# Performance work log

Hardware: AMD Instinct MI355X
Metric: run time of the kernel (lower is better)

Reference implementation:

```python
import jax, jax.numpy as jnp
import numpy as np

DIM, SSM, RNN = 1024, 64, 128


def setup_inputs() -> dict:
    key = jax.random.key(0)
    ks = jax.random.split(key, 16)
    s = 0.02
    B, N = 8, 2048
    return {
        'x': jax.random.normal(ks[0], (B, N, DIM), jnp.float32),
        'A': jax.random.normal(ks[1], (SSM, SSM), jnp.float32) * s,
        'Bw': jax.random.normal(ks[2], (SSM, DIM), jnp.float32) * s,
        'Bb': jnp.zeros((SSM,), jnp.float32),
        'Cw': jax.random.normal(ks[3], (DIM, SSM), jnp.float32) * s,
        'Cb': jnp.zeros((DIM,), jnp.float32),
        'Dw': jax.random.normal(ks[4], (DIM, DIM), jnp.float32) * s,
        'Db': jnp.zeros((DIM,), jnp.float32),
        'W_ih': jax.random.normal(ks[5], (3 * RNN, DIM), jnp.float32) * s,
        'b_ih': jnp.zeros((3 * RNN,), jnp.float32),
        'W_hh': jax.random.normal(ks[6], (3 * RNN, RNN), jnp.float32) * s,
        'b_hh': jnp.zeros((3 * RNN,), jnp.float32),
        'proj_w': jax.random.normal(ks[7], (DIM, RNN), jnp.float32) * s,
        'proj_b': jnp.zeros((DIM,), jnp.float32),
        'gate_w': jax.random.normal(ks[8], (2, DIM), jnp.float32) * s,
        'gate_b': jnp.zeros((2,), jnp.float32),
    }


def reference(x, A, Bw, Bb, Cw, Cb, Dw, Db, W_ih, b_ih, W_hh, b_hh, proj_w, proj_b, gate_w, gate_b):
    B, N, D = x.shape
    R = W_hh.shape[1]
    # Precompute all input-side projections once (time-parallel GEMMs).
    bx = jnp.einsum('bnd,sd->bns', x, Bw) + Bb            # [B,N,SSM]
    dx = jnp.einsum('bnd,ed->bne', x, Dw) + Db            # [B,N,D]
    gx = jax.nn.sigmoid(jnp.einsum('bnd,gd->bng', x, gate_w) + gate_b)  # [B,N,2]
    ih = jnp.einsum('bnd,rd->bnr', x, W_ih) + b_ih        # [B,N,3R]
    # time-major for scan
    bx_t = jnp.swapaxes(bx, 0, 1)
    dx_t = jnp.swapaxes(dx, 0, 1)
    gx_t = jnp.swapaxes(gx, 0, 1)
    ih_t = jnp.swapaxes(ih, 0, 1)

    h_ssm0 = jnp.zeros((B, A.shape[0]), x.dtype)
    h_rnn0 = jnp.zeros((B, R), x.dtype)

    def step(carry, inp):
        h_ssm, h_rnn = carry
        bxt, dxt, gxt, iht = inp
        h_ssm = jax.nn.silu(h_ssm @ A.T + bxt)
        y_ssm = h_ssm @ Cw.T + Cb + dxt
        # GRUCell (torch semantics)
        hh = h_rnn @ W_hh.T + b_hh
        i_r, i_z, i_n = jnp.split(iht, 3, axis=-1)
        h_r, h_z, h_n = jnp.split(hh, 3, axis=-1)
        r = jax.nn.sigmoid(i_r + h_r)
        z = jax.nn.sigmoid(i_z + h_z)
        n = jnp.tanh(i_n + r * h_n)
        h_rnn = (1.0 - z) * n + z * h_rnn
        y_rnn = h_rnn @ proj_w.T + proj_b
        fused = gxt[:, :1] * y_ssm + gxt[:, 1:2] * y_rnn
        return (h_ssm, h_rnn), fused

    _, out = jax.lax.scan(step, (h_ssm0, h_rnn0), (bx_t, dx_t, gx_t, ih_t))
    return jnp.swapaxes(out, 0, 1)  # [B,N,D]
```

## Files before the change

kernel.cpp:

```cpp
#include <hip/hip_runtime.h>


#define MROWS 16384
#define SEQ   2048
#define CH    16
#define NCH   (SEQ / CH)

typedef __attribute__((ext_vector_type(8))) short bf16x8;
typedef __attribute__((ext_vector_type(4))) float f32x4;

__device__ __forceinline__ float bf2f(unsigned short u) {
    union { unsigned int i; float f; } c; c.i = ((unsigned int)u) << 16; return c.f;
}
__device__ __forceinline__ unsigned short f2bf(float f) {
    union { float f; unsigned int i; } c; c.f = f;
    unsigned int x = c.i;
    return (unsigned short)((x + 0x7fffu + ((x >> 16) & 1u)) >> 16);
}
__device__ __forceinline__ unsigned int f2bf_pk(float lo, float hi) {
    unsigned int r;
    asm("v_cvt_pk_bf16_f32 %0, %1, %2" : "=v"(r) : "v"(lo), "v"(hi));
    return r;
}
__device__ __forceinline__ float ldin(const void* p, size_t i, int isf32) {
    return isf32 ? ((const float*)p)[i] : bf2f(((const unsigned short*)p)[i]);
}
__device__ __forceinline__ float sigf(float v) { return 1.f / (1.f + __expf(-v)); }
__device__ __forceinline__ float tanhf_fast(float v) { return 2.f * sigf(2.f * v) - 1.f; }

__global__ void sniff_kernel(const unsigned short* __restrict__ x, int* __restrict__ flag) {
    int tid = threadIdx.x;
    int big = 0;
    for (int i = tid; i < 1024; i += 64) {
        unsigned int e = (x[i] >> 7) & 0xFFu;
        big += (e >= 0xC0u) ? 1 : 0;
    }
#pragma unroll
    for (int off = 32; off; off >>= 1) big += __shfl_down(big, off);
    if (tid == 0) *flag = (big >= 4) ? 1 : 0;
}

__global__ void zero_out_kernel(float* __restrict__ out) {
    size_t i = ((size_t)blockIdx.x * 256 + threadIdx.x) * 16;
#pragma unroll
    for (int u = 0; u < 16; u++) out[i + u] = 0.f;
}

__device__ __forceinline__ void stage_tile(const void* __restrict__ g,
                                           int ld, int row0, int rowmax, int kb,
                                           short (*lds)[40], int tid, int isf32) {
#pragma unroll
    for (int q = 0; q < 2; q++) {
        int oct = q * 256 + tid;
        int row = oct >> 2, c8 = (oct & 3) << 3;
        int gr = row0 + row; if (gr > rowmax) gr = rowmax;
        size_t base = (size_t)gr * ld + kb + c8;
        bf16x8 v;
        if (isf32) {
            const float* gp = (const float*)g + base;
            float4 f0 = *reinterpret_cast<const float4*>(gp);
            float4 f1 = *reinterpret_cast<const float4*>(gp + 4);
            union { bf16x8 v8; unsigned int u[4]; } u;
            u.u[0] = f2bf_pk(f0.x, f0.y);
            u.u[1] = f2bf_pk(f0.z, f0.w);
            u.u[2] = f2bf_pk(f1.x, f1.y);
            u.u[3] = f2bf_pk(f1.z, f1.w);
            v = u.v8;
        } else {
            v = *reinterpret_cast<const bf16x8*>((const unsigned short*)g + base);
        }
        *reinterpret_cast<bf16x8*>(&lds[row][c8]) = v;
    }
}

__device__ __forceinline__ void mfma_tiles(const short (*As)[40], const short (*Bs)[40],
                                           int wm, int wn, int lane, f32x4 (*acc)[4]) {
    bf16x8 af[4], bfr[4];
    int m = lane & 15, ko = (lane >> 4) << 3;
#pragma unroll
    for (int i = 0; i < 4; i++)
        af[i] = *reinterpret_cast<const bf16x8*>(&As[wm + i * 16 + m][ko]);
#pragma unroll
    for (int j = 0; j < 4; j++)
        bfr[j] = *reinterpret_cast<const bf16x8*>(&Bs[wn + j * 16 + m][ko]);
#pragma unroll
    for (int i = 0; i < 4; i++)
#pragma unroll
        for (int j = 0; j < 4; j++)
            acc[i][j] = __builtin_amdgcn_mfma_f32_16x16x32_bf16(af[i], bfr[j], acc[i][j], 0, 0, 0);
}

__global__ __launch_bounds__(256) void gemm_bt_kernel(
    const void* __restrict__ A, const void* __restrict__ W,
    const void* __restrict__ bias, unsigned short* __restrict__ C,
    int M, int N, int K, const int* __restrict__ flagp) {
    __shared__ __align__(16) short As[128][40];
    __shared__ __align__(16) short Bs[128][40];
    int isf32 = *flagp;
    int tid = threadIdx.x, lane = tid & 63, wave = tid >> 6;
    int wm = (wave >> 1) << 6, wn = (wave & 1) << 6;
    int tileM = blockIdx.x << 7, tileN = blockIdx.y << 7;
    f32x4 acc[4][4];
    f32x4 z = {0.f, 0.f, 0.f, 0.f};
#pragma unroll
    for (int i = 0; i < 4; i++)
#pragma unroll
        for (int j = 0; j < 4; j++) acc[i][j] = z;

    for (int kb = 0; kb < K; kb += 32) {
        __syncthreads();
        stage_tile(A, K, tileM, M - 1, kb, As, tid, isf32);
        stage_tile(W, K, tileN, N - 1, kb, Bs, tid, isf32);
        __syncthreads();
        mfma_tiles(As, Bs, wm, wn, lane, acc);
    }
#pragma unroll
    for (int i = 0; i < 4; i++) {
#pragma unroll
        for (int j = 0; j < 4; j++) {
            int col = tileN + wn + j * 16 + (lane & 15);
            if (col < N) {
                float bv = ldin(bias, col, isf32);
                int row0 = tileM + wm + i * 16 + ((lane >> 4) << 2);
                unsigned int pk0 = f2bf_pk(acc[i][j][0] + bv, acc[i][j][1] + bv);
                unsigned int pk1 = f2bf_pk(acc[i][j][2] + bv, acc[i][j][3] + bv);
                C[(size_t)(row0 + 0) * N + col] = (unsigned short)(pk0 & 0xFFFFu);
                C[(size_t)(row0 + 1) * N + col] = (unsigned short)(pk0 >> 16);
                C[(size_t)(row0 + 2) * N + col] = (unsigned short)(pk1 & 0xFFFFu);
                C[(size_t)(row0 + 3) * N + col] = (unsigned short)(pk1 >> 16);
            }
        }
    }
}

__global__ __launch_bounds__(256) void gate_kernel(
    const void* __restrict__ x, const void* __restrict__ gw,
    const void* __restrict__ gb, float* __restrict__ gx, const int* __restrict__ flagp) {
    int isf32 = *flagp;
    int row = (blockIdx.x << 2) + (threadIdx.x >> 6);
    int lane = threadIdx.x & 63;
    size_t xoff = (size_t)row * 1024 + lane * 16;
    float a0 = 0.f, a1 = 0.f;
#pragma unroll
    for (int q = 0; q < 2; q++) {
#pragma unroll
        for (int e = 0; e < 8; e++) {
            size_t k = q * 8 + e;
            float xf = ldin(x, xoff + k, isf32);
            a0 += xf * ldin(gw, (size_t)lane * 16 + k, isf32);
            a1 += xf * ldin(gw, 1024 + (size_t)lane * 16 + k, isf32);
        }
    }
#pragma unroll
    for (int off = 32; off > 0; off >>= 1) {
        a0 += __shfl_down(a0, off);
        a1 += __shfl_down(a1, off);
    }
    if (lane == 0) {
        gx[row * 2]     = sigf(a0 + ldin(gb, 0, isf32));
        gx[row * 2 + 1] = sigf(a1 + ldin(gb, 1, isf32));
    }
}

__global__ __launch_bounds__(512) void scan_kernel(
    const void* __restrict__ Amat,
    const void* __restrict__ Whh,
    const void* __restrict__ bhh,
    const unsigned short* __restrict__ bxw,
    const unsigned short* __restrict__ ihw,
    unsigned short* __restrict__ hsw,
    unsigned short* __restrict__ hrw,
    const int* __restrict__ flagp) {
    int isf32 = *flagp;
    int b = blockIdx.x & 7;
    size_t rowbase = (size_t)b * SEQ;
    f32x4 zf = {0.f, 0.f, 0.f, 0.f};

    if (blockIdx.x < 8) {
        __shared__ __align__(16) unsigned short H[2][128];
        __shared__ __align__(16) unsigned short IH[2][CH][384];
        int tid = threadIdx.x, lane = tid & 63, w = tid >> 6;
        int col = lane & 15, quad = lane >> 4;
        int o = w * 16 + col;
        if (tid < 256) ((unsigned short*)H)[tid] = 0;
        bf16x8 Bf[3][4];
#pragma unroll
        for (int g = 0; g < 3; g++) {
            int n = g * 128 + o;
#pragma unroll
            for (int c = 0; c < 4; c++) {
                int k0 = c * 32 + quad * 8;
                bf16x8 v;
#pragma unroll
                for (int e = 0; e < 8; e++)
                    v[e] = (short)f2bf(ldin(Whh, (size_t)n * 128 + k0 + e, isf32));
                Bf[g][c] = v;
            }
        }
        float bias_r = ldin(bhh, o, isf32);
        float bias_z = ldin(bhh, 128 + o, isf32);
        float bias_n = ldin(bhh, 256 + o, isf32);
        float hprev = 0.f;
        bool gl = (quad == 0);
        const unsigned short* ihbase = ihw + rowbase * 384;
        bf16x8 stg0, stg1;
        stg0 = *reinterpret_cast<const bf16x8*>(ihbase + (size_t)tid * 8);
        if (tid < 256) stg1 = *reinterpret_cast<const bf16x8*>(ihbase + (size_t)(512 + tid) * 8);
        *reinterpret_cast<bf16x8*>(&IH[0][0][0] + (size_t)tid * 8) = stg0;
        if (tid < 256) *reinterpret_cast<bf16x8*>(&IH[0][0][0] + (size_t)(512 + tid) * 8) = stg1;
        stg0 = *reinterpret_cast<const bf16x8*>(ihbase + (size_t)CH * 384 + (size_t)tid * 8);
        if (tid < 256) stg1 = *reinterpret_cast<const bf16x8*>(ihbase + (size_t)CH * 384 + (size_t)(512 + tid) * 8);
        __syncthreads();

        int p = 0;
        for (int c = 0; c < NCH; c++) {
            int cur = c & 1;
            for (int tt = 0; tt < CH; tt++) {
                int t = c * CH + tt;
                bf16x8 Af[4];
#pragma unroll
                for (int cc = 0; cc < 4; cc++)
                    Af[cc] = *reinterpret_cast<const bf16x8*>(&H[p][cc * 32 + quad * 8]);
                float ir  = bf2f(IH[cur][tt][o]);
                float iz  = bf2f(IH[cur][tt][128 + o]);
                float inn = bf2f(IH[cur][tt][256 + o]);
                f32x4 accL[3], accH[3];
#pragma unroll
                for (int g = 0; g < 3; g++) { accL[g] = zf; accH[g] = zf; }
#pragma unroll
                for (int g = 0; g < 3; g++) {
                    accL[g] = __builtin_amdgcn_mfma_f32_16x16x32_bf16(Af[0], Bf[g][0], accL[g], 0, 0, 0);
                    accH[g] = __builtin_amdgcn_mfma_f32_16x16x32_bf16(Af[2], Bf[g][2], accH[g], 0, 0, 0);
                    accL[g] = __builtin_amdgcn_mfma_f32_16x16x32_bf16(Af[1], Bf[g][1], accL[g], 0, 0, 0);
                    accH[g] = __builtin_amdgcn_mfma_f32_16x16x32_bf16(Af[3], Bf[g][3], accH[g], 0, 0, 0);
                }
                float sr = accL[0][0] + accH[0][0];
                float sz = accL[1][0] + accH[1][0];
                float sn = accL[2][0] + accH[2][0];
                float r  = sigf(ir + sr + bias_r);
                float zg = sigf(iz + sz + bias_z);
                float n  = tanhf_fast(inn + r * (sn + bias_n));
                float hnew = (1.f - zg) * n + zg * hprev;
                hprev = hnew;
                if (gl) {
                    unsigned short hb = f2bf(hnew);
                    H[p ^ 1][o] = hb;
                    hrw[(rowbase + t) * 128 + o] = hb;
                }
                asm volatile("s_waitcnt lgkmcnt(0)" ::: "memory");
                __builtin_amdgcn_s_barrier();
                asm volatile("" ::: "memory");
                p ^= 1;
            }
            if (c + 1 < NCH) {
                unsigned short* dst = &IH[(c + 1) & 1][0][0];
                *reinterpret_cast<bf16x8*>(dst + (size_t)tid * 8) = stg0;
                if (tid < 256) *reinterpret_cast<bf16x8*>(dst + (size_t)(512 + tid) * 8) = stg1;
                if (c + 2 < NCH) {
                    const unsigned short* src = ihbase + (size_t)(c + 2) * CH * 384;
                    stg0 = *reinterpret_cast<const bf16x8*>(src + (size_t)tid * 8);
                    if (tid < 256) stg1 = *reinterpret_cast<const bf16x8*>(src + (size_t)(512 + tid) * 8);
                }
                asm volatile("s_waitcnt lgkmcnt(0)" ::: "memory");
                __builtin_amdgcn_s_barrier();
                asm volatile("" ::: "memory");
            }
        }
    } else {
        if (threadIdx.x >= 64) return;
        int lane = threadIdx.x, col = lane & 15, quad = lane >> 4;
        __shared__ __align__(16) unsigned short Hs[2][64];
        __shared__ __align__(16) unsigned short BX[2][CH][64];
        ((unsigned short*)Hs)[lane] = 0;
        ((unsigned short*)Hs)[64 + lane] = 0;
        bf16x8 Bf[4][2];
#pragma unroll
        for (int l = 0; l < 4; l++) {
            int n = l * 16 + col;
#pragma unroll
            for (int c = 0; c < 2; c++) {
                int k0 = c * 32 + quad * 8;
                bf16x8 v;
#pragma unroll
                for (int e = 0; e < 8; e++)
                    v[e] = (short)f2bf(ldin(Amat, (size_t)n * 64 + k0 + e, isf32));
                Bf[l][c] = v;
            }
        }
        bool gl = (quad == 0);
        const unsigned short* bxbase = bxw + rowbase * 64;
        bf16x8 stg[2];
#pragma unroll
        for (int q = 0; q < 2; q++)
            stg[q] = *reinterpret_cast<const bf16x8*>(bxbase + (size_t)(q * 64 + lane) * 8);
#pragma unroll
        for (int q = 0; q < 2; q++)
            *reinterpret_cast<bf16x8*>(&BX[0][0][0] + (size_t)(q * 64 + lane) * 8) = stg[q];
#pragma unroll
        for (int q = 0; q < 2; q++)
            stg[q] = *reinterpret_cast<const bf16x8*>(bxbase + (size_t)CH * 64 + (size_t)(q * 64 + lane) * 8);
        asm volatile("s_waitcnt lgkmcnt(0)" ::: "memory");

        int p = 0;
        for (int c = 0; c < NCH; c++) {
            int cur = c & 1;
            for (int tt = 0; tt < CH; tt++) {
                int t = c * CH + tt;
                bf16x8 Af[2];
#pragma unroll
                for (int cc = 0; cc < 2; cc++)
                    Af[cc] = *reinterpret_cast<const bf16x8*>(&Hs[p][cc * 32 + quad * 8]);
                float bx[4];
#pragma unroll
                for (int l = 0; l < 4; l++) bx[l] = bf2f(BX[cur][tt][l * 16 + col]);
                f32x4 acc[4];
#pragma unroll
                for (int l = 0; l < 4; l++) acc[l] = zf;
#pragma unroll
                for (int l = 0; l < 4; l++)
#pragma unroll
                    for (int cc = 0; cc < 2; cc++)
                        acc[l] = __builtin_amdgcn_mfma_f32_16x16x32_bf16(Af[cc], Bf[l][cc], acc[l], 0, 0, 0);
#pragma unroll
                for (int l = 0; l < 4; l++) {
                    int o = l * 16 + col;
                    float v = acc[l][0] + bx[l];
                    float hv = v * sigf(v);
                    unsigned short hb = f2bf(hv);
                    if (gl) {
                        Hs[p ^ 1][o] = hb;
                        hsw[(rowbase + t) * 64 + o] = hb;
                    }
                }
                asm volatile("s_waitcnt lgkmcnt(0)" ::: "memory");
                p ^= 1;
            }
            if (c + 1 < NCH) {
                unsigned short* dst = &BX[(c + 1) & 1][0][0];
#pragma unroll
                for (int q = 0; q < 2; q++)
                    *reinterpret_cast<bf16x8*>(dst + (size_t)(q * 64 + lane) * 8) = stg[q];
                if (c + 2 < NCH) {
#pragma unroll
                    for (int q = 0; q < 2; q++)
                        stg[q] = *reinterpret_cast<const bf16x8*>(
                            bxbase + (size_t)(c + 2) * CH * 64 + (size_t)(q * 64 + lane) * 8);
                }
                asm volatile("s_waitcnt lgkmcnt(0)" ::: "memory");
            }
        }
    }
}

__global__ __launch_bounds__(256) void out_kernel(
    const void* __restrict__ x,  const void* __restrict__ Dw, const void* __restrict__ Db,
    const unsigned short* __restrict__ hs, const void* __restrict__ Cw, const void* __restrict__ Cb,
    const unsigned short* __restrict__ hr, const void* __restrict__ pw, const void* __restrict__ pb,
    const float* __restrict__ gx, float* __restrict__ out,
    const int* __restrict__ flagp) {
    __shared__ __align__(16) short As[128][40];
    __shared__ __align__(16) short Bs[128][40];
    int isf32 = *flagp;
    int tid = threadIdx.x, lane = tid & 63, wave = tid >> 6;
    int wm = (wave >> 1) << 6, wn = (wave & 1) << 6;
    int tileM = blockIdx.x << 7, tileN = blockIdx.y << 7;
    f32x4 z = {0.f, 0.f, 0.f, 0.f};
    f32x4 acc1[4][4], acc2[4][4];
#pragma unroll
    for (int i = 0; i < 4; i++)
#pragma unroll
        for (int j = 0; j < 4; j++) { acc1[i][j] = z; acc2[i][j] = z; }

    for (int kb = 0; kb < 1024; kb += 32) {
        __syncthreads();
        stage_tile(x,  1024, tileM, MROWS - 1, kb, As, tid, isf32);
        stage_tile(Dw, 1024, tileN, 1023, kb, Bs, tid, isf32);
        __syncthreads();
        mfma_tiles(As, Bs, wm, wn, lane, acc1);
    }
    for (int kb = 0; kb < 64; kb += 32) {
        __syncthreads();
        stage_tile(hs, 64, tileM, MROWS - 1, kb, As, tid, 0);
        stage_tile(Cw, 64, tileN, 1023, kb, Bs, tid, isf32);
        __syncthreads();
        mfma_tiles(As, Bs, wm, wn, lane, acc1);
    }
    for (int kb = 0; kb < 128; kb += 32) {
        __syncthreads();
        stage_tile(hr, 128, tileM, MROWS - 1, kb, As, tid, 0);
        stage_tile(pw, 128, tileN, 1023, kb, Bs, tid, isf32);
        __syncthreads();
        mfma_tiles(As, Bs, wm, wn, lane, acc2);
    }
#pragma unroll
    for (int i = 0; i < 4; i++) {
        int r0 = tileM + wm + i * 16 + ((lane >> 4) << 2);
#pragma unroll
        for (int j = 0; j < 4; j++) {
            int col = tileN + wn + j * 16 + (lane & 15);
            float cb  = ldin(Cb, col, isf32) + ldin(Db, col, isf32);
            float pbv = ldin(pb, col, isf32);
#pragma unroll
            for (int r = 0; r < 4; r++) {
                int row = r0 + r;
                float g0 = gx[row * 2], g1 = gx[row * 2 + 1];
                out[(size_t)row * 1024 + col] =
                    g0 * (acc1[i][j][r] + cb) + g1 * (acc2[i][j][r] + pbv);
            }
        }
    }
}

extern "C" void kernel_launch(void* const* d_in, const int* in_sizes, int n_in,
                              void* d_out, int out_size, void* d_ws, size_t ws_size,
                              hipStream_t stream) {
    static const int expect_sizes[16] = {16777216, 4096, 65536, 64, 65536, 1024,
                                         1048576, 1024, 393216, 384, 49152, 384,
                                         131072, 1024, 2048, 2};
    bool order_ok = (n_in == 16);
    if (order_ok)
        for (int i = 0; i < 16; i++)
            if (in_sizes[i] != expect_sizes[i]) { order_ok = false; break; }
    float* out = (float*)d_out;
    if (!order_ok) {
        zero_out_kernel<<<dim3(4096), dim3(256), 0, stream>>>(out);
        return;
    }

    const void* x    = d_in[0];
    const void* Amat = d_in[1];
    const void* Bw   = d_in[2];
    const void* Bb   = d_in[3];
    const void* Cw   = d_in[4];
    const void* Cb   = d_in[5];
    const void* Dw   = d_in[6];
    const void* Db   = d_in[7];
    const void* Wih  = d_in[8];
    const void* bih  = d_in[9];
    const void* Whh  = d_in[10];
    const void* bhh  = d_in[11];
    const void* pw   = d_in[12];
    const void* pb   = d_in[13];
    const void* gw   = d_in[14];
    const void* gb   = d_in[15];

    char* ws = (char*)d_ws;
    int*            flg = (int*)(ws);
    float*          gxw = (float*)(ws + 256);
    unsigned short* hsw = (unsigned short*)(ws + 131328);
    unsigned short* hrw = (unsigned short*)(ws + 2228480);
    unsigned short* bxw = (unsigned short*)(ws + 6422784);
    unsigned short* ihw = (unsigned short*)(ws + 8519936);

    dim3 blk(256);
    sniff_kernel<<<dim3(1), dim3(64), 0, stream>>>((const unsigned short*)x, flg);
    gemm_bt_kernel<<<dim3(128, 3), blk, 0, stream>>>(x, Wih, bih, ihw, MROWS, 384, 1024, flg);
    gemm_bt_kernel<<<dim3(128, 1), blk, 0, stream>>>(x, Bw, Bb, bxw, MROWS, 64, 1024, flg);
    gate_kernel<<<dim3(4096), blk, 0, stream>>>(x, gw, gb, gxw, flg);
    scan_kernel<<<dim3(16), dim3(512), 0, stream>>>(Amat, Whh, bhh, bxw, ihw, hsw, hrw, flg);
    out_kernel<<<dim3(128, 8), blk, 0, stream>>>(x, Dw, Db, hsw, Cw, Cb, hrw, pw, pb, gxw, out, flg);
}
```

Before: 1.523 ms.

## Pre-convert inputs to bf16 once and spread scan chunk staging mid-chunk

Adds kernels that convert x and all weights and biases to bf16 once into workspace, so the GEMMs and the output kernel read half-width data instead of converting fp32 on every tile load. This path runs only when the workspace is large enough. In the scan, the refill of the next chunk's staging buffer now happens at step 8 inside the chunk loop, replacing the separate end-of-chunk store and barrier. MFMA issue is also wrapped in s_setprio. The conversion adds an extra pass over x, and the mid-chunk LDS write relies on the existing per-step barrier for correctness.

```diff
diff --git a/kernel.cpp b/kernel.cpp
--- a/kernel.cpp
+++ b/kernel.cpp
@@ -37,13 +37,74 @@
     }
 #pragma unroll
     for (int off = 32; off; off >>= 1) big += __shfl_down(big, off);
-    if (tid == 0) *flag = (big >= 4) ? 1 : 0;
+    if (tid == 0) { flag[0] = (big >= 4) ? 1 : 0; flag[1] = 0; }
 }
 
 __global__ void zero_out_kernel(float* __restrict__ out) {
     size_t i = ((size_t)blockIdx.x * 256 + threadIdx.x) * 16;
 #pragma unroll
     for (int u = 0; u < 16; u++) out[i + u] = 0.f;
+}
+
+__device__ __forceinline__ void cvt16(const void* src, unsigned short* dst,
+                                      size_t i0, int isf32) {
+#pragma unroll
+    for (int q = 0; q < 2; q++) {
+        size_t i = i0 + q * 8;
+        if (isf32) {
+            const float* s = (const float*)src + i;
+            float4 a = *reinterpret_cast<const float4*>(s);
+            float4 b = *reinterpret_cast<const float4*>(s + 4);
+            union { bf16x8 v; unsigned int u[4]; } u;
+            u.u[0] = f2bf_pk(a.x, a.y); u.u[1] = f2bf_pk(a.z, a.w);
+            u.u[2] = f2bf_pk(b.x, b.y); u.u[3] = f2bf_pk(b.z, b.w);
+            *reinterpret_cast<bf16x8*>(dst + i) = u.v;
+        } else {
+            *reinterpret_cast<bf16x8*>(dst + i) =
+                *reinterpret_cast<const bf16x8*>((const unsigned short*)src + i);
+        }
+    }
+}
+
+__global__ __launch_bounds__(256) void cvt_x_kernel(
+    const void* __restrict__ x, unsigned short* __restrict__ xb,
+    const int* __restrict__ flagp) {
+    int isf32 = *flagp;
+    size_t i0 = ((size_t)blockIdx.x * 256 + threadIdx.x) * 16;
+    cvt16(x, xb, i0, isf32);
+}
+
+__global__ __launch_bounds__(256) void cvt_w_kernel(
+    const void* __restrict__ Dw,  const void* __restrict__ Wih,
+    const void* __restrict__ pw,  const void* __restrict__ Cw,
+    const void* __restrict__ Bw,  const void* __restrict__ bih,
+    const void* __restrict__ Bb,  const void* __restrict__ Cb,
+    const void* __restrict__ Db,  const void* __restrict__ pb,
+    unsigned short* __restrict__ Dwb,  unsigned short* __restrict__ Wihb,
+    unsigned short* __restrict__ pwb,  unsigned short* __restrict__ Cwb,
+    unsigned short* __restrict__ Bwb,  unsigned short* __restrict__ bihb,
+    unsigned short* __restrict__ Bbb,  unsigned short* __restrict__ Cbb,
+    unsigned short* __restrict__ Dbb,  unsigned short* __restrict__ pbb,
+    const int* __restrict__ flagp) {
+    int isf32 = *flagp;
+    int blk = blockIdx.x, tid = threadIdx.x;
+    const void* src; unsigned short* dst; size_t base;
+    if (blk < 256)      { src = Dw;  dst = Dwb;  base = (size_t)blk * 4096; }
+    else if (blk < 352) { src = Wih; dst = Wihb; base = (size_t)(blk - 256) * 4096; }
+    else if (blk < 384) { src = pw;  dst = pwb;  base = (size_t)(blk - 352) * 4096; }
+    else if (blk < 400) { src = Cw;  dst = Cwb;  base = (size_t)(blk - 384) * 4096; }
+    else if (blk < 416) { src = Bw;  dst = Bwb;  base = (size_t)(blk - 400) * 4096; }
+    else {
+        for (int i = tid; i < 384; i += 256) bihb[i] = f2bf(ldin(bih, i, isf32));
+        if (tid < 64) Bbb[tid] = f2bf(ldin(Bb, tid, isf32));
+        for (int i = tid; i < 1024; i += 256) {
+            Cbb[i] = f2bf(ldin(Cb, i, isf32));
+            Dbb[i] = f2bf(ldin(Db, i, isf32));
+            pbb[i] = f2bf(ldin(pb, i, isf32));
+        }
+        return;
+    }
+    cvt16(src, dst, base + (size_t)tid * 16, isf32);
 }
 
 __device__ __forceinline__ void stage_tile(const void* __restrict__ g,
@@ -227,12 +288,26 @@
                 f32x4 accL[3], accH[3];
 #pragma unroll
                 for (int g = 0; g < 3; g++) { accL[g] = zf; accH[g] = zf; }
+                __builtin_amdgcn_s_setprio(1);
 #pragma unroll
                 for (int g = 0; g < 3; g++) {
                     accL[g] = __builtin_amdgcn_mfma_f32_16x16x32_bf16(Af[0], Bf[g][0], accL[g], 0, 0, 0);
                     accH[g] = __builtin_amdgcn_mfma_f32_16x16x32_bf16(Af[2], Bf[g][2], accH[g], 0, 0, 0);
                     accL[g] = __builtin_amdgcn_mfma_f32_16x16x32_bf16(Af[1], Bf[g][1], accL[g], 0, 0, 0);
                     accH[g] = __builtin_amdgcn_mfma_f32_16x16x32_bf16(Af[3], Bf[g][3], accH[g], 0, 0, 0);
+                }
+                __builtin_amdgcn_s_setprio(0);
+                if (tt == 8) {
+                    if (c + 1 < NCH) {
+                        unsigned short* dst = &IH[(c + 1) & 1][0][0];
+                        *reinterpret_cast<bf16x8*>(dst + (size_t)tid * 8) = stg0;
+                        if (tid < 256) *reinterpret_cast<bf16x8*>(dst + (size_t)(512 + tid) * 8) = stg1;
+                    }
+                    if (c + 2 < NCH) {
+                        const unsigned short* src = ihbase + (size_t)(c + 2) * CH * 384;
+                        stg0 = *reinterpret_cast<const bf16x8*>(src + (size_t)tid * 8);
+                        if (tid < 256) stg1 = *reinterpret_cast<const bf16x8*>(src + (size_t)(512 + tid) * 8);
+                    }
                 }
                 float sr = accL[0][0] + accH[0][0];
                 float sz = accL[1][0] + accH[1][0];
@@ -252,19 +327,6 @@
                 asm volatile("" ::: "memory");
                 p ^= 1;
             }
-            if (c + 1 < NCH) {
-                unsigned short* dst = &IH[(c + 1) & 1][0][0];
-                *reinterpret_cast<bf16x8*>(dst + (size_t)tid * 8) = stg0;
-                if (tid < 256) *reinterpret_cast<bf16x8*>(dst + (size_t)(512 + tid) * 8) = stg1;
-                if (c + 2 < NCH) {
-                    const unsigned short* src = ihbase + (size_t)(c + 2) * CH * 384;
-                    stg0 = *reinterpret_cast<const bf16x8*>(src + (size_t)tid * 8);
-                    if (tid < 256) stg1 = *reinterpret_cast<const bf16x8*>(src + (size_t)(512 + tid) * 8);
-                }
-                asm volatile("s_waitcnt lgkmcnt(0)" ::: "memory");
-                __builtin_amdgcn_s_barrier();
-                asm volatile("" ::: "memory");
-            }
         }
     } else {
         if (threadIdx.x >= 64) return;
@@ -321,6 +383,20 @@
 #pragma unroll
                     for (int cc = 0; cc < 2; cc++)
                         acc[l] = __builtin_amdgcn_mfma_f32_16x16x32_bf16(Af[cc], Bf[l][cc], acc[l], 0, 0, 0);
+                if (tt == 8) {
+                    if (c + 1 < NCH) {
+                        unsigned short* dst = &BX[(c + 1) & 1][0][0];
+#pragma unroll
+                        for (int q = 0; q < 2; q++)
+                            *reinterpret_cast<bf16x8*>(dst + (size_t)(q * 64 + lane) * 8) = stg[q];
+                    }
+                    if (c + 2 < NCH) {
+#pragma unroll
+                        for (int q = 0; q < 2; q++)
+                            stg[q] = *reinterpret_cast<const bf16x8*>(
+                                bxbase + (size_t)(c + 2) * CH * 64 + (size_t)(q * 64 + lane) * 8);
+                    }
+                }
 #pragma unroll
                 for (int l = 0; l < 4; l++) {
                     int o = l * 16 + col;
@@ -334,19 +410,6 @@
                 }
                 asm volatile("s_waitcnt lgkmcnt(0)" ::: "memory");
                 p ^= 1;
-            }
-            if (c + 1 < NCH) {
-                unsigned short* dst = &BX[(c + 1) & 1][0][0];
-#pragma unroll
-                for (int q = 0; q < 2; q++)
-                    *reinterpret_cast<bf16x8*>(dst + (size_t)(q * 64 + lane) * 8) = stg[q];
-                if (c + 2 < NCH) {
-#pragma unroll
-                    for (int q = 0; q < 2; q++)
-                        stg[q] = *reinterpret_cast<const bf16x8*>(
-                            bxbase + (size_t)(c + 2) * CH * 64 + (size_t)(q * 64 + lane) * 8);
-                }
-                asm volatile("s_waitcnt lgkmcnt(0)" ::: "memory");
             }
         }
     }
@@ -451,12 +514,36 @@
     unsigned short* hrw = (unsigned short*)(ws + 2228480);
     unsigned short* bxw = (unsigned short*)(ws + 6422784);
     unsigned short* ihw = (unsigned short*)(ws + 8519936);
+    unsigned short* xb   = (unsigned short*)(ws + 21102848);
+    unsigned short* Dwb  = (unsigned short*)(ws + 54657280);
+    unsigned short* Wihb = (unsigned short*)(ws + 56754432);
+    unsigned short* pwb  = (unsigned short*)(ws + 57540864);
+    unsigned short* Cwb  = (unsigned short*)(ws + 57803008);
+    unsigned short* Bwb  = (unsigned short*)(ws + 57934080);
+    unsigned short* bihb = (unsigned short*)(ws + 58065152);
+    unsigned short* Bbb  = (unsigned short*)(ws + 58069248);
+    unsigned short* Cbb  = (unsigned short*)(ws + 58073344);
+    unsigned short* Dbb  = (unsigned short*)(ws + 58077440);
+    unsigned short* pbb  = (unsigned short*)(ws + 58081536);
+    bool big = ws_size >= 58085632ull;
 
     dim3 blk(256);
     sniff_kernel<<<dim3(1), dim3(64), 0, stream>>>((const unsigned short*)x, flg);
-    gemm_bt_kernel<<<dim3(128, 3), blk, 0, stream>>>(x, Wih, bih, ihw, MROWS, 384, 1024, flg);
-    gemm_bt_kernel<<<dim3(128, 1), blk, 0, stream>>>(x, Bw, Bb, bxw, MROWS, 64, 1024, flg);
-    gate_kernel<<<dim3(4096), blk, 0, stream>>>(x, gw, gb, gxw, flg);
-    scan_kernel<<<dim3(16), dim3(512), 0, stream>>>(Amat, Whh, bhh, bxw, ihw, hsw, hrw, flg);
-    out_kernel<<<dim3(128, 8), blk, 0, stream>>>(x, Dw, Db, hsw, Cw, Cb, hrw, pw, pb, gxw, out, flg);
-}
+    if (big) {
+        cvt_x_kernel<<<dim3(4096), blk, 0, stream>>>(x, xb, flg);
+        cvt_w_kernel<<<dim3(417), blk, 0, stream>>>(
+            Dw, Wih, pw, Cw, Bw, bih, Bb, Cb, Db, pb,
+            Dwb, Wihb, pwb, Cwb, Bwb, bihb, Bbb, Cbb, Dbb, pbb, flg);
+        gemm_bt_kernel<<<dim3(128, 3), blk, 0, stream>>>(xb, Wihb, bihb, ihw, MROWS, 384, 1024, flg + 1);
+        gemm_bt_kernel<<<dim3(128, 1), blk, 0, stream>>>(xb, Bwb, Bbb, bxw, MROWS, 64, 1024, flg + 1);
+        gate_kernel<<<dim3(4096), blk, 0, stream>>>(x, gw, gb, gxw, flg);
+        scan_kernel<<<dim3(16), dim3(512), 0, stream>>>(Amat, Whh, bhh, bxw, ihw, hsw, hrw, flg);
+        out_kernel<<<dim3(128, 8), blk, 0, stream>>>(xb, Dwb, Dbb, hsw, Cwb, Cbb, hrw, pwb, pbb, gxw, out, flg + 1);
+    } else {
+        gemm_bt_kernel<<<dim3(128, 3), blk, 0, stream>>>(x, Wih, bih, ihw, MROWS, 384, 1024, flg);
+        gemm_bt_kernel<<<dim3(128, 1), blk, 0, stream>>>(x, Bw, Bb, bxw, MROWS, 64, 1024, flg);
+        gate_kernel<<<dim3(4096), blk, 0, stream>>>(x, gw, gb, gxw, flg);
+        scan_kernel<<<dim3(16), dim3(512), 0, stream>>>(Amat, Whh, bhh, bxw, ihw, hsw, hrw, flg);
+        out_kernel<<<dim3(128, 8), blk, 0, stream>>>(x, Dw, Db, hsw, Cw, Cb, hrw, pw, pb, gxw, out, flg);
+    }
+}
```

Result: faster. 1.447 ms (-5.0%).
